# Optimization experiments

Measured on AMD Instinct MI355X. Metric: run time of the kernel, lower is better.

The kernel has to match this reference:

```python
import jax, jax.numpy as jnp
import numpy as np

N_EMBD = 1024
N_STREAMS = 4
SK_ITERS = 20
SK_EPS = 1e-8


def setup_inputs() -> dict:
    key = jax.random.key(0)
    k_x, k_w = jax.random.split(key)
    B, T = 4, 4096
    D = N_STREAMS * N_EMBD
    x = jax.random.normal(k_x, (B, T, D), dtype=jnp.float32)
    # phi.weight: [n_streams^2, n_streams*n_embd], init std=0.01
    W = 0.01 * jax.random.normal(k_w, (N_STREAMS * N_STREAMS, D), dtype=jnp.float32)
    bias = 2.0 * jnp.eye(N_STREAMS, dtype=jnp.float32)  # [n, n]
    alpha = jnp.float32(0.01)
    return {"x": x, "W": W, "bias": bias, "alpha": alpha}


def _sinkhorn(H):
    # H: [..., n, n]; project exp(H) to doubly stochastic via Sinkhorn-Knopp
    M0 = jnp.exp(H)

    def body(_, M):
        M = M / (jnp.sum(M, axis=-2, keepdims=True) + SK_EPS)  # col normalize
        M = M / (jnp.sum(M, axis=-1, keepdims=True) + SK_EPS)  # row normalize
        return M

    return jax.lax.fori_loop(0, SK_ITERS, body, M0)


def reference(x, W, bias, alpha):
    B, T, D = x.shape
    n = N_STREAMS
    # RMSNorm over last dim (torch F.rms_norm default eps = dtype epsilon)
    eps = jnp.finfo(x.dtype).eps
    ms = jnp.mean(jnp.square(x), axis=-1, keepdims=True)
    x_norm = x * jax.lax.rsqrt(ms + eps)
    # phi (no bias): [B,T,D] @ [D, n*n] -> [B,T,n*n]
    dynamic = jnp.einsum('btd,nd->btn', x_norm, W).reshape(B, T, n, n)
    H_tilde = alpha * dynamic + bias  # bias [n,n] broadcasts
    return _sinkhorn(H_tilde)  # [B,T,n,n]
```

## Files before the change

kernel.cpp:

```cpp
#include <hip/hip_runtime.h>
#include <hip/hip_bf16.h>

#define DDIM 4096
#define NROWS 16384
#define SK_ITERS 20
#define KC 32
#define NCH 32

typedef __attribute__((ext_vector_type(8))) __bf16 bf16x8;
typedef __attribute__((ext_vector_type(4))) float f32x4;
typedef __attribute__((ext_vector_type(4))) int   i32x4;

__global__ __launch_bounds__(256, 4)
void rsm_kernel(const float* __restrict__ x, const float* __restrict__ W,
                const float* __restrict__ bias, const float* __restrict__ alpha_p,
                float* __restrict__ out)
{
    __shared__ __align__(16) float lds[4][4][16][KC];

    const int tid  = threadIdx.x;
    const int wave = tid >> 6;
    const int lane = tid & 63;
    const int r16  = lane & 15;
    const int kq   = lane >> 4;
    const int z    = r16 & 7;
    const int rowbase = blockIdx.x * 16;

    const float* sbase[2];
#pragma unroll
    for (int j = 0; j < 2; ++j) {
        int row = j * 8 + (lane >> 3);
        sbase[j] = x + (size_t)(rowbase + row) * DDIM + wave * 1024
                 + (((lane & 7) ^ (lane >> 3)) << 2);
    }

    const float* wq = W + (size_t)r16 * DDIM + wave * 1024 + kq * 8;

    i32x4 wr[4][2];

    auto issue = [&](int c) {
        const float* p = wq + c * KC;
        asm volatile(
            "global_load_dwordx4 %0, %2, off\n\t"
            "global_load_dwordx4 %1, %2, off offset:16"
            : "=&v"(wr[c & 3][0]), "=&v"(wr[c & 3][1])
            : "v"(p));
#pragma unroll
        for (int j = 0; j < 2; ++j) {
            __builtin_amdgcn_global_load_lds(
                (const __attribute__((address_space(1))) void*)(sbase[j] + c * KC),
                (__attribute__((address_space(3))) void*)(&lds[wave][c & 3][j * 8][0]),
                16, 0, 0);
        }
    };

    issue(0);
    issue(1);
    issue(2);

    f32x4 acc = {0.f, 0.f, 0.f, 0.f};
    float sumsq = 0.f;

#pragma unroll
    for (int c = 0; c < NCH; ++c) {
        if (c + 3 < NCH) issue(c + 3);
        __builtin_amdgcn_sched_barrier(0);
        if (c + 3 < NCH)      asm volatile("s_waitcnt vmcnt(12)" ::: "memory");
        else if (c == NCH - 3) asm volatile("s_waitcnt vmcnt(8)" ::: "memory");
        else if (c == NCH - 2) asm volatile("s_waitcnt vmcnt(4)" ::: "memory");
        else                   asm volatile("s_waitcnt vmcnt(0)" ::: "memory");
        __builtin_amdgcn_sched_barrier(0);

        const float* arow = &lds[wave][c & 3][r16][0];
        f32x4 a0 = *(const f32x4*)(arow + (((kq * 2    ) ^ z) << 2));
        f32x4 a1 = *(const f32x4*)(arow + (((kq * 2 + 1) ^ z) << 2));

        sumsq += a0[0]*a0[0] + a0[1]*a0[1] + a0[2]*a0[2] + a0[3]*a0[3]
               + a1[0]*a1[0] + a1[1]*a1[1] + a1[2]*a1[2] + a1[3]*a1[3];

        f32x4 b0 = __builtin_bit_cast(f32x4, wr[c & 3][0]);
        f32x4 b1 = __builtin_bit_cast(f32x4, wr[c & 3][1]);

        bf16x8 af, bv;
        af[0]=(__bf16)a0[0]; af[1]=(__bf16)a0[1]; af[2]=(__bf16)a0[2]; af[3]=(__bf16)a0[3];
        af[4]=(__bf16)a1[0]; af[5]=(__bf16)a1[1]; af[6]=(__bf16)a1[2]; af[7]=(__bf16)a1[3];
        bv[0]=(__bf16)b0[0]; bv[1]=(__bf16)b0[1]; bv[2]=(__bf16)b0[2]; bv[3]=(__bf16)b0[3];
        bv[4]=(__bf16)b1[0]; bv[5]=(__bf16)b1[1]; bv[6]=(__bf16)b1[2]; bv[7]=(__bf16)b1[3];

        acc = __builtin_amdgcn_mfma_f32_16x16x32_bf16(af, bv, acc, 0, 0, 0);
    }

    __syncthreads();
    float* sc = &lds[0][0][0][0];
    *(f32x4*)(sc + wave * 256 + lane * 4) = acc;
    sc[1024 + wave * 64 + lane] = sumsq;
    __syncthreads();

    if (wave == 0) {
        f32x4 cg = *(const f32x4*)(sc + lane * 4);
#pragma unroll
        for (int w = 1; w < 4; ++w)
            cg += *(const f32x4*)(sc + w * 256 + lane * 4);

        float s = sc[1024 + lane] + sc[1024 + 64 + lane]
                + sc[1024 + 128 + lane] + sc[1024 + 192 + lane];
        s += __shfl_xor(s, 16);
        s += __shfl_xor(s, 32);

        const float al = alpha_p[0];
        const float bi = bias[r16];

        float m[4];
#pragma unroll
        for (int r = 0; r < 4; ++r) {
            float Srow  = __shfl(s, kq * 4 + r);
            float scale = rsqrtf(Srow * (1.0f / DDIM) + 1.1920929e-07f);
            m[r] = expf(al * (cg[r] * scale) + bi);
        }

        for (int it = 0; it < SK_ITERS; ++it) {
#pragma unroll
            for (int r = 0; r < 4; ++r) {
                float t = m[r] + __shfl_xor(m[r], 4);
                t += __shfl_xor(t, 8);
                m[r] = m[r] / (t + 1e-8f);
            }
#pragma unroll
            for (int r = 0; r < 4; ++r) {
                float t = m[r] + __shfl_xor(m[r], 1);
                t += __shfl_xor(t, 2);
                m[r] = m[r] / (t + 1e-8f);
            }
        }

#pragma unroll
        for (int r = 0; r < 4; ++r)
            out[(size_t)(rowbase + kq * 4 + r) * 16 + r16] = m[r];
    }
}

extern "C" void kernel_launch(void* const* d_in, const int* in_sizes, int n_in,
                              void* d_out, int out_size, void* d_ws, size_t ws_size,
                              hipStream_t stream) {
    const float* x     = (const float*)d_in[0];
    const float* W     = (const float*)d_in[1];
    const float* bias  = (const float*)d_in[2];
    const float* alpha = (const float*)d_in[3];
    float* out = (float*)d_out;

    rsm_kernel<<<dim3(NROWS / 16), dim3(256), 0, stream>>>(x, W, bias, alpha, out);
}
```

Baseline: 53.16 us.

## Load full contiguous x rows per wave into shared LDS chunks with block barriers

Each wave now fetches whole 1 KB contiguous segments of 4 rows per chunk into a shared LDS buffer, instead of each wave owning a private quarter of the K dimension with 128-byte pieces. Every wave then reads its own K slice from the shared buffer, with two MFMAs per chunk and 16 chunks. The aim is longer contiguous global reads and fewer, larger chunks. In exchange it adds two workgroup barriers per iteration, doubles the LDS footprint, and lowers the launch-bounds occupancy hint.

```diff
diff --git a/kernel.cpp b/kernel.cpp
--- a/kernel.cpp
+++ b/kernel.cpp
@@ -4,19 +4,19 @@
 #define DDIM 4096
 #define NROWS 16384
 #define SK_ITERS 20
-#define KC 32
-#define NCH 32
+#define KC 256
+#define NCH 16
 
 typedef __attribute__((ext_vector_type(8))) __bf16 bf16x8;
 typedef __attribute__((ext_vector_type(4))) float f32x4;
 typedef __attribute__((ext_vector_type(4))) int   i32x4;
 
-__global__ __launch_bounds__(256, 4)
+__global__ __launch_bounds__(256, 2)
 void rsm_kernel(const float* __restrict__ x, const float* __restrict__ W,
                 const float* __restrict__ bias, const float* __restrict__ alpha_p,
                 float* __restrict__ out)
 {
-    __shared__ __align__(16) float lds[4][4][16][KC];
+    __shared__ __align__(16) float lds[4][16][KC];
 
     const int tid  = threadIdx.x;
     const int wave = tid >> 6;
@@ -26,30 +26,32 @@
     const int z    = r16 & 7;
     const int rowbase = blockIdx.x * 16;
 
-    const float* sbase[2];
+    const float* sbase[4];
 #pragma unroll
-    for (int j = 0; j < 2; ++j) {
-        int row = j * 8 + (lane >> 3);
-        sbase[j] = x + (size_t)(rowbase + row) * DDIM + wave * 1024
-                 + (((lane & 7) ^ (lane >> 3)) << 2);
+    for (int jj = 0; jj < 4; ++jj) {
+        int row = wave * 4 + jj;
+        sbase[jj] = x + (size_t)(rowbase + row) * DDIM + ((lane ^ (row & 7)) << 2);
     }
 
-    const float* wq = W + (size_t)r16 * DDIM + wave * 1024 + kq * 8;
+    const float* wq = W + (size_t)r16 * DDIM + wave * 64 + kq * 8;
 
-    i32x4 wr[4][2];
+    i32x4 wr[4][4];
 
     auto issue = [&](int c) {
         const float* p = wq + c * KC;
+        i32x4* wd = wr[c & 3];
         asm volatile(
-            "global_load_dwordx4 %0, %2, off\n\t"
-            "global_load_dwordx4 %1, %2, off offset:16"
-            : "=&v"(wr[c & 3][0]), "=&v"(wr[c & 3][1])
+            "global_load_dwordx4 %0, %4, off\n\t"
+            "global_load_dwordx4 %1, %4, off offset:16\n\t"
+            "global_load_dwordx4 %2, %4, off offset:128\n\t"
+            "global_load_dwordx4 %3, %4, off offset:144"
+            : "=&v"(wd[0]), "=&v"(wd[1]), "=&v"(wd[2]), "=&v"(wd[3])
             : "v"(p));
 #pragma unroll
-        for (int j = 0; j < 2; ++j) {
+        for (int jj = 0; jj < 4; ++jj) {
             __builtin_amdgcn_global_load_lds(
-                (const __attribute__((address_space(1))) void*)(sbase[j] + c * KC),
-                (__attribute__((address_space(3))) void*)(&lds[wave][c & 3][j * 8][0]),
+                (const __attribute__((address_space(1))) void*)(sbase[jj] + c * KC),
+                (__attribute__((address_space(3))) void*)(&lds[c & 3][wave * 4 + jj][0]),
                 16, 0, 0);
         }
     };
@@ -65,33 +67,42 @@
     for (int c = 0; c < NCH; ++c) {
         if (c + 3 < NCH) issue(c + 3);
         __builtin_amdgcn_sched_barrier(0);
-        if (c + 3 < NCH)      asm volatile("s_waitcnt vmcnt(12)" ::: "memory");
-        else if (c == NCH - 3) asm volatile("s_waitcnt vmcnt(8)" ::: "memory");
-        else if (c == NCH - 2) asm volatile("s_waitcnt vmcnt(4)" ::: "memory");
-        else                   asm volatile("s_waitcnt vmcnt(0)" ::: "memory");
+        if (c + 3 < NCH)       asm volatile("s_waitcnt vmcnt(24)" ::: "memory");
+        else if (c == NCH - 3) asm volatile("s_waitcnt vmcnt(16)" ::: "memory");
+        else if (c == NCH - 2) asm volatile("s_waitcnt vmcnt(8)"  ::: "memory");
+        else                   asm volatile("s_waitcnt vmcnt(0)"  ::: "memory");
+        __builtin_amdgcn_sched_barrier(0);
+        asm volatile("s_barrier" ::: "memory");
         __builtin_amdgcn_sched_barrier(0);
 
-        const float* arow = &lds[wave][c & 3][r16][0];
-        f32x4 a0 = *(const f32x4*)(arow + (((kq * 2    ) ^ z) << 2));
-        f32x4 a1 = *(const f32x4*)(arow + (((kq * 2 + 1) ^ z) << 2));
+        const float* arow = &lds[c & 3][r16][0];
+#pragma unroll
+        for (int st = 0; st < 2; ++st) {
+            const int g0 = wave * 16 + st * 8 + kq * 2;
+            f32x4 a0 = *(const f32x4*)(arow + (((g0    ) ^ z) << 2));
+            f32x4 a1 = *(const f32x4*)(arow + (((g0 + 1) ^ z) << 2));
 
-        sumsq += a0[0]*a0[0] + a0[1]*a0[1] + a0[2]*a0[2] + a0[3]*a0[3]
-               + a1[0]*a1[0] + a1[1]*a1[1] + a1[2]*a1[2] + a1[3]*a1[3];
+            sumsq += a0[0]*a0[0] + a0[1]*a0[1] + a0[2]*a0[2] + a0[3]*a0[3]
+                   + a1[0]*a1[0] + a1[1]*a1[1] + a1[2]*a1[2] + a1[3]*a1[3];
 
-        f32x4 b0 = __builtin_bit_cast(f32x4, wr[c & 3][0]);
-        f32x4 b1 = __builtin_bit_cast(f32x4, wr[c & 3][1]);
+            f32x4 b0 = __builtin_bit_cast(f32x4, wr[c & 3][st * 2]);
+            f32x4 b1 = __builtin_bit_cast(f32x4, wr[c & 3][st * 2 + 1]);
 
-        bf16x8 af, bv;
-        af[0]=(__bf16)a0[0]; af[1]=(__bf16)a0[1]; af[2]=(__bf16)a0[2]; af[3]=(__bf16)a0[3];
-        af[4]=(__bf16)a1[0]; af[5]=(__bf16)a1[1]; af[6]=(__bf16)a1[2]; af[7]=(__bf16)a1[3];
-        bv[0]=(__bf16)b0[0]; bv[1]=(__bf16)b0[1]; bv[2]=(__bf16)b0[2]; bv[3]=(__bf16)b0[3];
-        bv[4]=(__bf16)b1[0]; bv[5]=(__bf16)b1[1]; bv[6]=(__bf16)b1[2]; bv[7]=(__bf16)b1[3];
+            bf16x8 af, bv;
+            af[0]=(__bf16)a0[0]; af[1]=(__bf16)a0[1]; af[2]=(__bf16)a0[2]; af[3]=(__bf16)a0[3];
+            af[4]=(__bf16)a1[0]; af[5]=(__bf16)a1[1]; af[6]=(__bf16)a1[2]; af[7]=(__bf16)a1[3];
+            bv[0]=(__bf16)b0[0]; bv[1]=(__bf16)b0[1]; bv[2]=(__bf16)b0[2]; bv[3]=(__bf16)b0[3];
+            bv[4]=(__bf16)b1[0]; bv[5]=(__bf16)b1[1]; bv[6]=(__bf16)b1[2]; bv[7]=(__bf16)b1[3];
 
-        acc = __builtin_amdgcn_mfma_f32_16x16x32_bf16(af, bv, acc, 0, 0, 0);
+            acc = __builtin_amdgcn_mfma_f32_16x16x32_bf16(af, bv, acc, 0, 0, 0);
+        }
+
+        __builtin_amdgcn_sched_barrier(0);
+        asm volatile("s_barrier" ::: "memory");
     }
 
     __syncthreads();
-    float* sc = &lds[0][0][0][0];
+    float* sc = &lds[0][0][0];
     *(f32x4*)(sc + wave * 256 + lane * 4) = acc;
     sc[1024 + wave * 64 + lane] = sumsq;
     __syncthreads();
```

Result: slower. 67.86 us (+27.6%).

## Spread Sinkhorn epilogue across all four waves with fast reciprocal and exp

Applied to the files above, without the earlier changes.

The epilogue used to run on wave 0 only, with each lane holding four matrix entries. Now all 256 threads each own one of the 16x16 output entries and reduce the partial accumulators from LDS themselves. The sum-of-squares is reduced within each wave before it is stored, and exp and divide are replaced by __expf and hardware rcp. This shortens the serial Sinkhorn tail per block and gives contiguous output stores, at the cost of slightly lower precision in exp and the reciprocal.

```diff
diff --git a/kernel.cpp b/kernel.cpp
--- a/kernel.cpp
+++ b/kernel.cpp
@@ -65,7 +65,7 @@
     for (int c = 0; c < NCH; ++c) {
         if (c + 3 < NCH) issue(c + 3);
         __builtin_amdgcn_sched_barrier(0);
-        if (c + 3 < NCH)      asm volatile("s_waitcnt vmcnt(12)" ::: "memory");
+        if (c + 3 < NCH)       asm volatile("s_waitcnt vmcnt(12)" ::: "memory");
         else if (c == NCH - 3) asm volatile("s_waitcnt vmcnt(8)" ::: "memory");
         else if (c == NCH - 2) asm volatile("s_waitcnt vmcnt(4)" ::: "memory");
         else                   asm volatile("s_waitcnt vmcnt(0)" ::: "memory");
@@ -93,50 +93,34 @@
     __syncthreads();
     float* sc = &lds[0][0][0][0];
     *(f32x4*)(sc + wave * 256 + lane * 4) = acc;
-    sc[1024 + wave * 64 + lane] = sumsq;
+    float sq = sumsq;
+    sq += __shfl_xor(sq, 16);
+    sq += __shfl_xor(sq, 32);
+    if (lane < 16) sc[1024 + wave * 16 + lane] = sq;
     __syncthreads();
 
-    if (wave == 0) {
-        f32x4 cg = *(const f32x4*)(sc + lane * 4);
-#pragma unroll
-        for (int w = 1; w < 4; ++w)
-            cg += *(const f32x4*)(sc + w * 256 + lane * 4);
+    const int tr  = tid >> 4;
+    const int c16 = tid & 15;
+    const int ca  = (tr >> 2) * 64 + c16 * 4 + (tr & 3);
 
-        float s = sc[1024 + lane] + sc[1024 + 64 + lane]
-                + sc[1024 + 128 + lane] + sc[1024 + 192 + lane];
-        s += __shfl_xor(s, 16);
-        s += __shfl_xor(s, 32);
+    float cg = sc[ca] + sc[256 + ca] + sc[512 + ca] + sc[768 + ca];
+    float S  = sc[1024 + tr] + sc[1024 + 16 + tr]
+             + sc[1024 + 32 + tr] + sc[1024 + 48 + tr];
 
-        const float al = alpha_p[0];
-        const float bi = bias[r16];
+    float scale = rsqrtf(S * (1.0f / DDIM) + 1.1920929e-07f);
+    float h = alpha_p[0] * (cg * scale) + bias[c16];
+    float m = __expf(h);
 
-        float m[4];
-#pragma unroll
-        for (int r = 0; r < 4; ++r) {
-            float Srow  = __shfl(s, kq * 4 + r);
-            float scale = rsqrtf(Srow * (1.0f / DDIM) + 1.1920929e-07f);
-            m[r] = expf(al * (cg[r] * scale) + bi);
-        }
+    for (int it = 0; it < SK_ITERS; ++it) {
+        float t1 = m + __shfl_xor(m, 4);
+        t1 += __shfl_xor(t1, 8);
+        m = m * __builtin_amdgcn_rcpf(t1 + 1e-8f);
+        float t2 = m + __shfl_xor(m, 1);
+        t2 += __shfl_xor(t2, 2);
+        m = m * __builtin_amdgcn_rcpf(t2 + 1e-8f);
+    }
 
-        for (int it = 0; it < SK_ITERS; ++it) {
-#pragma unroll
-            for (int r = 0; r < 4; ++r) {
-                float t = m[r] + __shfl_xor(m[r], 4);
-                t += __shfl_xor(t, 8);
-                m[r] = m[r] / (t + 1e-8f);
-            }
-#pragma unroll
-            for (int r = 0; r < 4; ++r) {
-                float t = m[r] + __shfl_xor(m[r], 1);
-                t += __shfl_xor(t, 2);
-                m[r] = m[r] / (t + 1e-8f);
-            }
-        }
-
-#pragma unroll
-        for (int r = 0; r < 4; ++r)
-            out[(size_t)(rowbase + kq * 4 + r) * 16 + r16] = m[r];
-    }
+    out[(size_t)rowbase * 16 + tid] = m;
 }
 
 extern "C" void kernel_launch(void* const* d_in, const int* in_sizes, int n_in,
```

New measurement: 48.45 us. -8.9%, faster.
